# Performance work log

Hardware: AMD Instinct MI355X
Metric: run time of the kernel (lower is better)

## Reference

```python
import jax, jax.numpy as jnp
import numpy as np

H = 8          # num heads
HD = 64        # head dim
DV = 512       # values_dim
DC = 128       # coords_dim
DI = 512       # att_inner_dim
DF = 2048      # mlp inner dim


def _ln(x, g, b, eps=1e-5):
    mu = jnp.mean(x, -1, keepdims=True)
    var = jnp.mean((x - mu) ** 2, -1, keepdims=True)
    return (x - mu) * jax.lax.rsqrt(var + eps) * g + b


def _rms(x, g, eps=1e-6):
    return x * jax.lax.rsqrt(jnp.mean(x * x, -1, keepdims=True) + eps) * g


def _heads(x):  # b n (h d) -> b h n d
    b, n, _ = x.shape
    return x.reshape(b, n, H, HD).transpose(0, 2, 1, 3)


def setup_inputs() -> dict:
    key = jax.random.key(0)
    ks = iter(jax.random.split(key, 40))
    r = lambda shape, s=0.02: jax.random.normal(next(ks), shape, jnp.float32) * s
    inp = {
        'coords': jax.random.normal(next(ks), (4, 4096, DC), jnp.float32),
        'values': jax.random.normal(next(ks), (4, 4096, DV), jnp.float32),
        'Lv': jax.random.normal(next(ks), (4, 1024, DV), jnp.float32),
        'Lc': jax.random.normal(next(ks), (4, 1024, DC), jnp.float32),
        'lam': jax.random.normal(next(ks), (1,), jnp.float32),
        'lvn_g': jnp.ones((DV,)), 'lvn_b': jnp.zeros((DV,)),
        'lcn_g': jnp.ones((DC,)), 'lcn_b': jnp.zeros((DC,)),
        'ck_w': r((DC, DI)), 'ck_b': jnp.zeros((DI,)), 'ck_g': jnp.ones((DI,)),
        'cq_w': r((DC, DI)), 'cq_b': jnp.zeros((DI,)), 'cq_g': jnp.ones((DI,)),
        'vq_w': r((DV, DI)), 'vq_b': jnp.zeros((DI,)), 'vq_g': jnp.ones((DI,)),
        'vk_w': r((DV, 2 * DI)), 'vk_b': jnp.zeros((2 * DI,)),
        'op_w': r((DI, DV)), 'op_b': jnp.zeros((DV,)),
        'oln_g': jnp.ones((DV,)), 'oln_b': jnp.zeros((DV,)),
        'm1_w': r((DV, DF)), 'm1_b': jnp.zeros((DF,)),
        'm2_w': r((DF, DF)), 'm2_b': jnp.zeros((DF,)),
        'm3_w': r((DF, DV)), 'm3_b': jnp.zeros((DV,)),
    }
    return inp


def reference(coords, values, Lv, Lc, lam, lvn_g, lvn_b, lcn_g, lcn_b,
              ck_w, ck_b, ck_g, cq_w, cq_b, cq_g, vq_w, vq_b, vq_g,
              vk_w, vk_b, op_w, op_b, oln_g, oln_b,
              m1_w, m1_b, m2_w, m2_b, m3_w, m3_b):
    Lv = _ln(Lv, lvn_g, lvn_b)
    Lc = _ln(Lc, lcn_g, lcn_b)
    vk = Lv @ vk_w + vk_b                     # [b, nl, 2*DI]
    v_v, k_v = jnp.split(vk, 2, axis=-1)
    k_c = _rms(Lc @ ck_w + ck_b, ck_g)
    k_c, v_v, k_v = _heads(k_c), _heads(v_v), _heads(k_v)  # [b,h,nl,d]
    q_v = _heads(_rms(values @ vq_w + vq_b, vq_g))         # [b,h,nq,d]
    q_c = _heads(_rms(coords @ cq_w + cq_b, cq_g))
    # dual-score attention
    scores = jnp.einsum('bhnd,bhmd->bhnm', q_c, k_c) \
        + lam[0] * jnp.einsum('bhnd,bhmd->bhnm', q_v, k_v)
    scores = scores / np.float32(np.sqrt(HD))
    attn = jax.nn.softmax(scores, axis=-1)
    V_out = jnp.einsum('bhnm,bhmd->bhnd', attn, v_v)       # [b,h,nq,d]
    b, _, nq, _ = V_out.shape
    V_out = V_out.transpose(0, 2, 1, 3).reshape(b, nq, DI)
    V_out = V_out @ op_w + op_b
    # (LayerNorm, MLP) head: Linear-GELU-Linear-GELU-Linear
    h = _ln(V_out, oln_g, oln_b)
    h = jax.nn.gelu(h @ m1_w + m1_b)
    h = jax.nn.gelu(h @ m2_w + m2_b)
    return h @ m3_w + m3_b
```

## Files before the change

### kernel.cpp

```cpp
#include <hip/hip_runtime.h>
#include <cstdint>
#include <cstddef>

typedef __bf16 bf16_t;
typedef __bf16 bf16x8 __attribute__((ext_vector_type(8)));
typedef __bf16 bf16x4 __attribute__((ext_vector_type(4)));
typedef __bf16 bf16x2 __attribute__((ext_vector_type(2)));
typedef float  f32x4  __attribute__((ext_vector_type(4)));

typedef __attribute__((address_space(1))) void gvoid_t;
typedef __attribute__((address_space(3))) void lvoid_t;

__device__ __forceinline__ f32x4 mfma16(bf16x8 a, bf16x8 b, f32x4 c) {
  return __builtin_amdgcn_mfma_f32_16x16x32_bf16(a, b, c, 0, 0, 0);
}

__device__ __forceinline__ void async_copy16(const void* g, void* l) {
  __builtin_amdgcn_global_load_lds((gvoid_t*)g, (lvoid_t*)l, 16, 0, 0);
}

__device__ __forceinline__ float gelu_tanh(float x) {
  float u = 0.7978845608028654f * (x + 0.044715f * x * x * x);
  float e = exp2f(2.8853900817779268f * u);
  float t = 1.f - 2.f / (e + 1.f);
  return 0.5f * x * (1.f + t);
}

struct TransBatch {
  const float* src[8];
  bf16_t* dst[8];
  int K[8], N[8], bx[8], base[8];
};

__global__ void transpose_batch_kernel(TransBatch d) {
  int id = blockIdx.x;
  int mi = 0;
#pragma unroll
  for (int j = 1; j < 8; j++)
    if (id >= d.base[j]) mi = j;
  int local = id - d.base[mi];
  int bxw = d.bx[mi];
  int n0 = (local % bxw) * 32, k0 = (local / bxw) * 32;
  const float* in = d.src[mi];
  bf16_t* out = d.dst[mi];
  int K = d.K[mi], N = d.N[mi];

  __shared__ float t[32][33];
  int tx = threadIdx.x, ty = threadIdx.y;
#pragma unroll
  for (int i = 0; i < 4; i++)
    t[ty + i * 8][tx] = in[(size_t)(k0 + ty + i * 8) * N + n0 + tx];
  __syncthreads();
#pragma unroll
  for (int i = 0; i < 4; i++)
    out[(size_t)(n0 + ty + i * 8) * K + k0 + tx] = (bf16_t)t[tx][ty + i * 8];
}

__global__ void transpose_v_kernel(const bf16_t* __restrict__ vk, bf16_t* __restrict__ vt) {
  __shared__ bf16_t t[32][33];
  int b = blockIdx.z;
  int d0 = blockIdx.x * 32, m0 = blockIdx.y * 32;
  int tx = threadIdx.x, ty = threadIdx.y;
#pragma unroll
  for (int i = 0; i < 4; i++)
    t[ty + i * 8][tx] = vk[((size_t)b * 1024 + m0 + ty + i * 8) * 1024 + d0 + tx];
  __syncthreads();
#pragma unroll
  for (int i = 0; i < 4; i++)
    vt[((size_t)b * 512 + d0 + ty + i * 8) * 1024 + m0 + tx] = t[tx][ty + i * 8];
}

__global__ void cvt2_bf16_kernel(const float* __restrict__ a, bf16_t* __restrict__ oa, int n4a,
                                 const float* __restrict__ b, bf16_t* __restrict__ ob, int n4b) {
  int i = blockIdx.x * blockDim.x + threadIdx.x;
  const float* s;
  bf16_t* o;
  int j;
  if (i < n4a) { s = a; o = oa; j = i; }
  else { j = i - n4a; if (j >= n4b) return; s = b; o = ob; }
  float4 v = ((const float4*)s)[j];
  bf16x4 r = {(bf16_t)v.x, (bf16_t)v.y, (bf16_t)v.z, (bf16_t)v.w};
  ((bf16x4*)o)[j] = r;
}

template <int D, bool IS_RMS, typename TI>
__global__ __launch_bounds__(256) void rownorm_kernel(
    const TI* __restrict__ x, const float* __restrict__ g,
    const float* __restrict__ bb, bf16_t* __restrict__ out) {
  constexpr int V = D / 64;
  const int row = blockIdx.x * 4 + (threadIdx.x >> 6);
  const int lane = threadIdx.x & 63;
  const size_t base = (size_t)row * D + (size_t)lane * V;
  float v[V];
  if constexpr (sizeof(TI) == 2) {
    bf16x8 xv = *(const bf16x8*)(x + base);
#pragma unroll
    for (int j = 0; j < V; j++) v[j] = (float)xv[j];
  } else if constexpr (V == 8) {
    float4 a = ((const float4*)(x + base))[0];
    float4 b2 = ((const float4*)(x + base))[1];
    v[0] = a.x; v[1] = a.y; v[2] = a.z; v[3] = a.w;
    v[4] = b2.x; v[5] = b2.y; v[6] = b2.z; v[7] = b2.w;
  } else {
    float2 a = *(const float2*)(x + base);
    v[0] = a.x; v[1] = a.y;
  }
  float s = 0.f, s2 = 0.f;
#pragma unroll
  for (int j = 0; j < V; j++) { s += v[j]; s2 += v[j] * v[j]; }
#pragma unroll
  for (int o = 32; o > 0; o >>= 1) { s += __shfl_xor(s, o); s2 += __shfl_xor(s2, o); }
  float mu, rr;
  if constexpr (IS_RMS) {
    mu = 0.f;
    rr = rsqrtf(s2 * (1.f / D) + 1e-6f);
  } else {
    mu = s * (1.f / D);
    rr = rsqrtf(s2 * (1.f / D) - mu * mu + 1e-5f);
  }
  float o[V];
#pragma unroll
  for (int j = 0; j < V; j++) {
    float gv = g[lane * V + j];
    float bv;
    if constexpr (IS_RMS) bv = 0.f; else bv = bb[lane * V + j];
    o[j] = (v[j] - mu) * rr * gv + bv;
  }
  if constexpr (V == 8) {
    bf16x8 ov;
#pragma unroll
    for (int j = 0; j < 8; j++) ov[j] = (bf16_t)o[j];
    *(bf16x8*)(out + base) = ov;
  } else {
    bf16x2 ov;
    ov[0] = (bf16_t)o[0]; ov[1] = (bf16_t)o[1];
    *(bf16x2*)(out + base) = ov;
  }
}

template <int EPI>
__global__ __launch_bounds__(256, 2) void gemm_bt(
    const bf16_t* __restrict__ A, const bf16_t* __restrict__ Bt,
    const float* __restrict__ bias, void* __restrict__ outp,
    int M, int N, int K) {
  __shared__ __align__(16) bf16_t As[128 * 64];
  __shared__ __align__(16) bf16_t Bs[128 * 64];
  const int tid = threadIdx.x;
  const int lane = tid & 63, wv = tid >> 6;
  const int quad = lane >> 4, l16 = lane & 15;
  int nwg = gridDim.x * gridDim.y;
  int bid = blockIdx.y * gridDim.x + blockIdx.x;
  if (!(nwg & 7)) { int cpx = nwg >> 3; bid = (bid & 7) * cpx + (bid >> 3); }
  const int m_base = (bid / gridDim.x) * 128, n_base = (bid % gridDim.x) * 128;
  const int wm = wv & 1, wn = wv >> 1;
  f32x4 acc[4][4] = {};

  for (int k0 = 0; k0 < K; k0 += 64) {
#pragma unroll
    for (int c = 0; c < 4; c++) {
      int p = c * 256 + tid;
      int row = p >> 3;
      int gc = (p & 7) ^ (row & 7);
      async_copy16(&A[(size_t)(m_base + row) * K + k0 + gc * 8], &As[(size_t)p * 8]);
      async_copy16(&Bt[(size_t)(n_base + row) * K + k0 + gc * 8], &Bs[(size_t)p * 8]);
    }
    __syncthreads();
#pragma unroll
    for (int ks = 0; ks < 2; ks++) {
      bf16x8 af[4], bfr[4];
#pragma unroll
      for (int mi = 0; mi < 4; mi++) {
        int r = wm * 64 + mi * 16 + l16;
        int c = (ks * 4 + quad) ^ (r & 7);
        af[mi] = *(const bf16x8*)&As[(size_t)(r * 8 + c) * 8];
      }
#pragma unroll
      for (int ni = 0; ni < 4; ni++) {
        int r = wn * 64 + ni * 16 + l16;
        int c = (ks * 4 + quad) ^ (r & 7);
        bfr[ni] = *(const bf16x8*)&Bs[(size_t)(r * 8 + c) * 8];
      }
#pragma unroll
      for (int mi = 0; mi < 4; mi++)
#pragma unroll
        for (int ni = 0; ni < 4; ni++)
          acc[mi][ni] = mfma16(af[mi], bfr[ni], acc[mi][ni]);
    }
    __syncthreads();
  }

#pragma unroll
  for (int mi = 0; mi < 4; mi++) {
    int m = m_base + wm * 64 + mi * 16 + quad * 4;
#pragma unroll
    for (int ni = 0; ni < 4; ni++) {
      int n = n_base + wn * 64 + ni * 16 + l16;
      float bv = bias[n];
#pragma unroll
      for (int r2 = 0; r2 < 4; r2++) {
        float v = acc[mi][ni][r2] + bv;
        if (EPI == 2) v = gelu_tanh(v);
        if (EPI == 0) ((float*)outp)[(size_t)(m + r2) * N + n] = v;
        else          ((bf16_t*)outp)[(size_t)(m + r2) * N + n] = (bf16_t)v;
      }
    }
  }
}

#define SCHED_FENCE() __builtin_amdgcn_sched_barrier(0)

#define PHT(MM) \
  SCHED_FENCE(); \
  asm volatile("s_waitcnt lgkmcnt(0)" ::: "memory"); \
  SCHED_FENCE(); \
  __builtin_amdgcn_s_setprio(1); \
  MM; \
  __builtin_amdgcn_s_setprio(0); \
  SCHED_FENCE(); \
  __builtin_amdgcn_s_barrier(); \
  SCHED_FENCE();

#define PHT_VM(MM) \
  SCHED_FENCE(); \
  asm volatile("s_waitcnt lgkmcnt(0)" ::: "memory"); \
  SCHED_FENCE(); \
  __builtin_amdgcn_s_setprio(1); \
  MM; \
  __builtin_amdgcn_s_setprio(0); \
  SCHED_FENCE(); \
  asm volatile("s_waitcnt vmcnt(6)" ::: "memory"); \
  __builtin_amdgcn_s_barrier(); \
  SCHED_FENCE();

template <int EPI>
__global__ __launch_bounds__(512, 2) void gemm256(
    const bf16_t* __restrict__ A, const bf16_t* __restrict__ Bt,
    const float* __restrict__ bias, void* __restrict__ outp,
    int M, int N, int K) {
  __shared__ __align__(16) bf16_t As[2][256 * 64];
  __shared__ __align__(16) bf16_t Bs[2][256 * 64];
  const int tid = threadIdx.x;
  const int lane = tid & 63, wid = tid >> 6;
  const int quad = lane >> 4, l16 = lane & 15, l7 = l16 & 7;
  const int wm = wid >> 2, wn = wid & 3;
  int nwg = gridDim.x * gridDim.y;
  int bid = blockIdx.y * gridDim.x + blockIdx.x;
  if (!(nwg & 7)) { int cpx = nwg >> 3; bid = (bid & 7) * cpx + (bid >> 3); }
  const int m_base = (bid / gridDim.x) * 256, n_base = (bid % gridDim.x) * 256;
  const int nkt = K >> 6, nit = nkt >> 1;

  f32x4 acc[8][4] = {};

  const bf16_t* aB[2], * bB[2];
#pragma unroll
  for (int ks = 0; ks < 2; ks++) {
    aB[ks] = &As[0][0] + (wm * 128 + l16) * 64 + (((ks * 4 + quad) ^ l7)) * 8;
    bB[ks] = &Bs[0][0] + (wn * 64 + l16) * 64 + (((ks * 4 + quad) ^ l7)) * 8;
  }
  auto ldA = [&](int buf, int rg, bf16x8 (&af)[2][2]) {
#pragma unroll
    for (int mi = 0; mi < 2; mi++)
#pragma unroll
      for (int ks = 0; ks < 2; ks++)
        af[mi][ks] = *(const bf16x8*)(aB[ks] + buf * 16384 + rg * 2048 + mi * 1024);
  };
  auto ldB = [&](int buf, bf16x8 (&bfr)[4][2]) {
#pragma unroll
    for (int cf = 0; cf < 4; cf++)
#pragma unroll
      for (int ks = 0; ks < 2; ks++)
        bfr[cf][ks] = *(const bf16x8*)(bB[ks] + buf * 16384 + cf * 1024);
  };
  auto mm = [&](int rg, bf16x8 (&a)[2][2], bf16x8 (&b)[4][2]) {
#pragma unroll
    for (int ks = 0; ks < 2; ks++)
#pragma unroll
      for (int mi = 0; mi < 2; mi++)
#pragma unroll
        for (int cf = 0; cf < 4; cf++)
          acc[rg * 2 + mi][cf] = mfma16(a[mi][ks], b[cf][ks], acc[rg * 2 + mi][cf]);
  };

  const int rr = tid >> 3;
  const int cb = ((tid & 7) ^ (rr & 7)) * 16;
  const char* pa00 = (const char*)A + 2 * ((size_t)(m_base + 0 + rr) * K) + cb;
  const char* pa01 = (const char*)A + 2 * ((size_t)(m_base + 64 + rr) * K) + cb;
  const char* pa10 = (const char*)A + 2 * ((size_t)(m_base + 128 + rr) * K) + cb;
  const char* pa11 = (const char*)A + 2 * ((size_t)(m_base + 192 + rr) * K) + cb;
  const char* pb00 = (const char*)Bt + 2 * ((size_t)(n_base + 0 + rr) * K) + cb;
  const char* pb01 = (const char*)Bt + 2 * ((size_t)(n_base + 64 + rr) * K) + cb;
  const char* pb10 = (const char*)Bt + 2 * ((size_t)(n_base + 128 + rr) * K) + cb;
  const char* pb11 = (const char*)Bt + 2 * ((size_t)(n_base + 192 + rr) * K) + cb;
  bf16_t* dA0 = &As[0][0] + tid * 8;
  bf16_t* dB0 = &Bs[0][0] + tid * 8;
  auto stage = [&](const char*& p0, const char*& p1, bf16_t* d0) {
    async_copy16(p0, d0);
    async_copy16(p1, d0 + 4096);
    p0 += 128; p1 += 128;
  };

  stage(pb00, pb01, dB0);
  stage(pb10, pb11, dB0 + 8192);
  stage(pa00, pa01, dA0);
  stage(pa10, pa11, dA0 + 8192);
  stage(pb00, pb01, dB0 + 16384);
  stage(pb10, pb11, dB0 + 16384 + 8192);
  stage(pa00, pa01, dA0 + 16384);
  asm volatile("s_waitcnt vmcnt(6)" ::: "memory");
  SCHED_FENCE();
  __builtin_amdgcn_s_barrier();
  SCHED_FENCE();

  bf16x8 af[2][2], afn[2][2], bfr[4][2];
  for (int it = 0; it < nit; ++it) {
    ldB(0, bfr); ldA(0, 0, af);
    stage(pa10, pa11, dA0 + 16384 + 8192);
    PHT(mm(0, af, bfr));
    ldA(0, 1, af);
    stage(pb00, pb01, dB0);
    PHT(mm(1, af, bfr));
    ldA(0, 2, af); ldA(0, 3, afn);
    stage(pb10, pb11, dB0 + 8192);
    PHT(mm(2, af, bfr));
    stage(pa00, pa01, dA0);
    PHT_VM(mm(3, afn, bfr));
    ldB(1, bfr); ldA(1, 0, af);
    stage(pa10, pa11, dA0 + 8192);
    PHT(mm(0, af, bfr));
    ldA(1, 1, af);
    stage(pb00, pb01, dB0 + 16384);
    PHT(mm(1, af, bfr));
    ldA(1, 2, af); ldA(1, 3, afn);
    stage(pb10, pb11, dB0 + 16384 + 8192);
    PHT(mm(2, af, bfr));
    stage(pa00, pa01, dA0 + 16384);
    PHT_VM(mm(3, afn, bfr));
  }
  asm volatile("s_waitcnt vmcnt(0)" ::: "memory");

#pragma unroll
  for (int rf = 0; rf < 8; rf++) {
    int m = m_base + wm * 128 + rf * 16 + quad * 4;
#pragma unroll
    for (int cf = 0; cf < 4; cf++) {
      int n = n_base + wn * 64 + cf * 16 + l16;
      float bv = bias[n];
#pragma unroll
      for (int r2 = 0; r2 < 4; r2++) {
        float v = acc[rf][cf][r2] + bv;
        if (EPI == 2) v = gelu_tanh(v);
        if (EPI == 0) ((float*)outp)[(size_t)(m + r2) * N + n] = v;
        else          ((bf16_t*)outp)[(size_t)(m + r2) * N + n] = (bf16_t)v;
      }
    }
  }
}

template <int EPI>
__global__ __launch_bounds__(256, 2) void gemm64(
    const bf16_t* __restrict__ A, const bf16_t* __restrict__ Bt,
    const float* __restrict__ bias, void* __restrict__ outp,
    int M, int N, int K) {
  __shared__ __align__(16) bf16_t As[64 * 32];
  __shared__ __align__(16) bf16_t Bs[128 * 32];
  const int tid = threadIdx.x;
  const int lane = tid & 63, wv = tid >> 6;
  const int quad = lane >> 4, l16 = lane & 15;
  const int m_base = blockIdx.y * 64, n_base = blockIdx.x * 128;
  const int wm = wv & 1, wn = wv >> 1;
  f32x4 acc[2][4] = {};

  for (int k0 = 0; k0 < K; k0 += 32) {
    {
      int p = tid;
      int row = p >> 2;
      int kc = (p & 3) ^ ((row >> 1) & 3);
      async_copy16(&A[(size_t)(m_base + row) * K + k0 + kc * 8], &As[(size_t)p * 8]);
    }
#pragma unroll
    for (int c = 0; c < 2; c++) {
      int p = c * 256 + tid;
      int row = p >> 2;
      int kc = (p & 3) ^ ((row >> 1) & 3);
      async_copy16(&Bt[(size_t)(n_base + row) * K + k0 + kc * 8], &Bs[(size_t)p * 8]);
    }
    __syncthreads();
    bf16x8 af[2], bfr[4];
#pragma unroll
    for (int mi = 0; mi < 2; mi++) {
      int r = wm * 32 + mi * 16 + l16;
      int kc = quad ^ ((r >> 1) & 3);
      af[mi] = *(const bf16x8*)&As[(size_t)(r * 4 + kc) * 8];
    }
#pragma unroll
    for (int ni = 0; ni < 4; ni++) {
      int r = wn * 64 + ni * 16 + l16;
      int kc = quad ^ ((r >> 1) & 3);
      bfr[ni] = *(const bf16x8*)&Bs[(size_t)(r * 4 + kc) * 8];
    }
#pragma unroll
    for (int mi = 0; mi < 2; mi++)
#pragma unroll
      for (int ni = 0; ni < 4; ni++)
        acc[mi][ni] = mfma16(af[mi], bfr[ni], acc[mi][ni]);
    __syncthreads();
  }

#pragma unroll
  for (int mi = 0; mi < 2; mi++) {
    int m = m_base + wm * 32 + mi * 16 + quad * 4;
#pragma unroll
    for (int ni = 0; ni < 4; ni++) {
      int n = n_base + wn * 64 + ni * 16 + l16;
      float bv = bias[n];
#pragma unroll
      for (int r2 = 0; r2 < 4; r2++) {
        float v = acc[mi][ni][r2] + bv;
        if (EPI == 2) v = gelu_tanh(v);
        if (EPI == 0) ((float*)outp)[(size_t)(m + r2) * N + n] = v;
        else          ((bf16_t*)outp)[(size_t)(m + r2) * N + n] = (bf16_t)v;
      }
    }
  }
}

__global__ __launch_bounds__(256, 2) void attn_kernel(
    const bf16_t* __restrict__ qc, const bf16_t* __restrict__ qv,
    const bf16_t* __restrict__ kcb, const bf16_t* __restrict__ vkb,
    const bf16_t* __restrict__ vt, const float* __restrict__ lamp,
    bf16_t* __restrict__ vout) {
  const int b = blockIdx.z, h = blockIdx.y;
  const int tid = threadIdx.x;
  const int lane = tid & 63, wv = tid >> 6;
  const int quad = lane >> 4, l16 = lane & 15;
  const int qrow0 = blockIdx.x * 128 + wv * 32;
  const float SCL = 0.125f * 1.4426950408889634f;
  const float C1 = SCL, C2 = lamp[0] * SCL;

  __shared__ __align__(16) bf16_t kcS[64 * 64];
  __shared__ __align__(16) bf16_t kvS[64 * 64];
  __shared__ __align__(16) bf16_t vtS[64 * 64];
  __shared__ __align__(16) bf16_t sP[4][32 * 64];
  bf16_t* sPw = sP[wv];

  bf16x8 qcf[2][2], qvf[2][2];
#pragma unroll
  for (int mt = 0; mt < 2; mt++)
#pragma unroll
    for (int ks = 0; ks < 2; ks++) {
      size_t o = ((size_t)b * 4096 + qrow0 + mt * 16 + l16) * 512 + h * 64 + ks * 32 + quad * 8;
      qcf[mt][ks] = *(const bf16x8*)&qc[o];
      qvf[mt][ks] = *(const bf16x8*)&qv[o];
    }

  f32x4 O[2][4] = {};
  float ls[2][4] = {};

  for (int kb = 0; kb < 16; kb++) {
#pragma unroll
    for (int i = 0; i < 2; i++) {
      int p = i * 256 + tid;
      int row = p >> 3;
      int gc = (p & 7) ^ (row & 7);
      async_copy16(&kcb[((size_t)b * 1024 + kb * 64 + row) * 512 + h * 64 + gc * 8],
                   &kcS[(size_t)p * 8]);
      async_copy16(&vkb[((size_t)b * 1024 + kb * 64 + row) * 1024 + 512 + h * 64 + gc * 8],
                   &kvS[(size_t)p * 8]);
      async_copy16(&vt[((size_t)((b * 8 + h) * 64) + row) * 1024 + kb * 64 + gc * 8],
                   &vtS[(size_t)p * 8]);
    }
    __syncthreads();

#pragma unroll
    for (int nt = 0; nt < 4; nt++) {
      int krow = nt * 16 + l16;
      int kb8 = krow & 7;
      bf16x8 kc0 = *(const bf16x8*)&kcS[(size_t)(krow * 8 + (quad ^ kb8)) * 8];
      bf16x8 kc1 = *(const bf16x8*)&kcS[(size_t)(krow * 8 + ((4 + quad) ^ kb8)) * 8];
      bf16x8 kv0 = *(const bf16x8*)&kvS[(size_t)(krow * 8 + (quad ^ kb8)) * 8];
      bf16x8 kv1 = *(const bf16x8*)&kvS[(size_t)(krow * 8 + ((4 + quad) ^ kb8)) * 8];
#pragma unroll
      for (int mt = 0; mt < 2; mt++) {
        f32x4 sc = {};
        sc = mfma16(qcf[mt][0], kc0, sc);
        sc = mfma16(qcf[mt][1], kc1, sc);
        f32x4 sv = {};
        sv = mfma16(qvf[mt][0], kv0, sv);
        sv = mfma16(qvf[mt][1], kv1, sv);
#pragma unroll
        for (int r = 0; r < 4; r++) {
          float p = exp2f(sc[r] * C1 + sv[r] * C2);
          ls[mt][r] += p;
          int prow = mt * 16 + quad * 4 + r;
          int col = nt * 16 + l16;
          sPw[prow * 64 + (((col >> 3) ^ (prow & 7)) * 8) + (col & 7)] = (bf16_t)p;
        }
      }
    }
    asm volatile("s_waitcnt lgkmcnt(0)" ::: "memory");

#pragma unroll
    for (int ks2 = 0; ks2 < 2; ks2++) {
      bf16x8 pa[2];
#pragma unroll
      for (int mt = 0; mt < 2; mt++) {
        int prow = mt * 16 + l16;
        pa[mt] = *(const bf16x8*)&sPw[(size_t)(prow * 8 + ((ks2 * 4 + quad) ^ (prow & 7))) * 8];
      }
#pragma unroll
      for (int ntd = 0; ntd < 4; ntd++) {
        int drow = ntd * 16 + l16;
        bf16x8 vb = *(const bf16x8*)&vtS[(size_t)(drow * 8 + ((ks2 * 4 + quad) ^ (drow & 7))) * 8];
        O[0][ntd] = mfma16(pa[0], vb, O[0][ntd]);
        O[1][ntd] = mfma16(pa[1], vb, O[1][ntd]);
      }
    }
    __syncthreads();
  }

#pragma unroll
  for (int mt = 0; mt < 2; mt++) {
    float inv[4];
#pragma unroll
    for (int r = 0; r < 4; r++) {
      float v = ls[mt][r];
      v += __shfl_xor(v, 1);
      v += __shfl_xor(v, 2);
      v += __shfl_xor(v, 4);
      v += __shfl_xor(v, 8);
      inv[r] = 1.f / v;
    }
#pragma unroll
    for (int ntd = 0; ntd < 4; ntd++)
#pragma unroll
      for (int r = 0; r < 4; r++) {
        size_t o = ((size_t)b * 4096 + qrow0 + mt * 16 + quad * 4 + r) * 512 + h * 64 + ntd * 16 + l16;
        vout[o] = (bf16_t)(O[mt][ntd][r] * inv[r]);
      }
  }
}

extern "C" void kernel_launch(void* const* d_in, const int* in_sizes, int n_in,
                              void* d_out, int out_size, void* d_ws, size_t ws_size,
                              hipStream_t stream) {
  (void)in_sizes; (void)n_in; (void)out_size; (void)ws_size;
  const float* coords = (const float*)d_in[0];
  const float* values = (const float*)d_in[1];
  const float* Lv     = (const float*)d_in[2];
  const float* Lc     = (const float*)d_in[3];
  const float* lam    = (const float*)d_in[4];
  const float* lvn_g  = (const float*)d_in[5];
  const float* lvn_b  = (const float*)d_in[6];
  const float* lcn_g  = (const float*)d_in[7];
  const float* lcn_b  = (const float*)d_in[8];
  const float* ck_w = (const float*)d_in[9];  const float* ck_b = (const float*)d_in[10]; const float* ck_g = (const float*)d_in[11];
  const float* cq_w = (const float*)d_in[12]; const float* cq_b = (const float*)d_in[13]; const float* cq_g = (const float*)d_in[14];
  const float* vq_w = (const float*)d_in[15]; const float* vq_b = (const float*)d_in[16]; const float* vq_g = (const float*)d_in[17];
  const float* vk_w = (const float*)d_in[18]; const float* vk_b = (const float*)d_in[19];
  const float* op_w = (const float*)d_in[20]; const float* op_b = (const float*)d_in[21];
  const float* oln_g = (const float*)d_in[22]; const float* oln_b = (const float*)d_in[23];
  const float* m1_w = (const float*)d_in[24]; const float* m1_b = (const float*)d_in[25];
  const float* m2_w = (const float*)d_in[26]; const float* m2_b = (const float*)d_in[27];
  const float* m3_w = (const float*)d_in[28]; const float* m3_b = (const float*)d_in[29];

  char* ws = (char*)d_ws;
  size_t off = 0;
  auto alloc = [&](size_t bytes) { void* p = ws + off; off += (bytes + 255) & ~(size_t)255; return p; };

  bf16_t* wt_m1 = (bf16_t*)alloc((size_t)512 * 2048 * 2);
  bf16_t* wt_m2 = (bf16_t*)alloc((size_t)2048 * 2048 * 2);
  bf16_t* wt_m3 = (bf16_t*)alloc((size_t)2048 * 512 * 2);
  bf16_t* scr0  = (bf16_t*)alloc((size_t)16384 * 512 * 4);
  bf16_t* qv_bf = (bf16_t*)alloc((size_t)16384 * 512 * 2);
  bf16_t* qc_bf = (bf16_t*)alloc((size_t)16384 * 512 * 2);
  bf16_t* voutb = (bf16_t*)alloc((size_t)16384 * 512 * 2);
  bf16_t* h0    = (bf16_t*)alloc((size_t)16384 * 512 * 2);
  bf16_t* h1    = (bf16_t*)alloc((size_t)16384 * 2048 * 2);
  bf16_t* h2    = (bf16_t*)alloc((size_t)16384 * 2048 * 2);

  size_t ov = (size_t)((char*)h1 - ws);
  auto oalloc = [&](size_t bytes) { void* p = ws + ov; ov += (bytes + 255) & ~(size_t)255; return p; };
  bf16_t* wt_vk = (bf16_t*)oalloc((size_t)1024 * 512 * 2);
  bf16_t* wt_ck = (bf16_t*)oalloc((size_t)512 * 128 * 2);
  bf16_t* wt_cq = (bf16_t*)oalloc((size_t)512 * 128 * 2);
  bf16_t* wt_vq = (bf16_t*)oalloc((size_t)512 * 512 * 2);
  bf16_t* wt_op = (bf16_t*)oalloc((size_t)512 * 512 * 2);
  bf16_t* lv_ln = (bf16_t*)oalloc((size_t)4096 * 512 * 2);
  bf16_t* lc_ln = (bf16_t*)oalloc((size_t)4096 * 128 * 2);
  bf16_t* vkob  = (bf16_t*)oalloc((size_t)4096 * 1024 * 2);
  bf16_t* kc_b  = (bf16_t*)oalloc((size_t)4096 * 512 * 2);
  bf16_t* kc_bf = (bf16_t*)oalloc((size_t)4096 * 512 * 2);
  bf16_t* val_bf= (bf16_t*)oalloc((size_t)16384 * 512 * 2);
  bf16_t* crd_bf= (bf16_t*)oalloc((size_t)16384 * 128 * 2);
  bf16_t* vt    = (bf16_t*)oalloc((size_t)4 * 512 * 1024 * 2);

  TransBatch tb8;
  const float* srcs[8] = {vk_w, ck_w, cq_w, vq_w, op_w, m1_w, m2_w, m3_w};
  bf16_t* dsts[8] = {wt_vk, wt_ck, wt_cq, wt_vq, wt_op, wt_m1, wt_m2, wt_m3};
  int Ks[8] = {512, 128, 128, 512, 512, 512, 2048, 2048};
  int Ns[8] = {1024, 512, 512, 512, 512, 2048, 2048, 512};
  int cum = 0;
  for (int i = 0; i < 8; i++) {
    tb8.src[i] = srcs[i]; tb8.dst[i] = dsts[i];
    tb8.K[i] = Ks[i]; tb8.N[i] = Ns[i];
    tb8.bx[i] = Ns[i] / 32;
    tb8.base[i] = cum;
    cum += (Ns[i] / 32) * (Ks[i] / 32);
  }
  transpose_batch_kernel<<<cum, dim3(32, 8), 0, stream>>>(tb8);

  cvt2_bf16_kernel<<<(16384 * 512 / 4 + 16384 * 128 / 4 + 255) / 256, 256, 0, stream>>>(
      values, val_bf, 16384 * 512 / 4, coords, crd_bf, 16384 * 128 / 4);

  rownorm_kernel<512, false, float><<<1024, 256, 0, stream>>>(Lv, lvn_g, lvn_b, lv_ln);
  rownorm_kernel<128, false, float><<<1024, 256, 0, stream>>>(Lc, lcn_g, lcn_b, lc_ln);

  gemm_bt<1><<<dim3(8, 32), 256, 0, stream>>>(lv_ln, wt_vk, vk_b, vkob, 4096, 1024, 512);
  gemm64<1><<<dim3(4, 64), 256, 0, stream>>>(lc_ln, wt_ck, ck_b, kc_b, 4096, 512, 128);
  rownorm_kernel<512, true, bf16_t><<<1024, 256, 0, stream>>>(kc_b, ck_g, nullptr, kc_bf);

  gemm_bt<1><<<dim3(4, 128), 256, 0, stream>>>(val_bf, wt_vq, vq_b, scr0, 16384, 512, 512);
  rownorm_kernel<512, true, bf16_t><<<4096, 256, 0, stream>>>(scr0, vq_g, nullptr, qv_bf);
  gemm64<1><<<dim3(4, 256), 256, 0, stream>>>(crd_bf, wt_cq, cq_b, scr0, 16384, 512, 128);
  rownorm_kernel<512, true, bf16_t><<<4096, 256, 0, stream>>>(scr0, cq_g, nullptr, qc_bf);

  transpose_v_kernel<<<dim3(16, 32, 4), dim3(32, 8), 0, stream>>>(vkob, vt);

  attn_kernel<<<dim3(32, 8, 4), 256, 0, stream>>>(qc_bf, qv_bf, kc_bf, vkob, vt, lam, voutb);

  gemm_bt<1><<<dim3(4, 128), 256, 0, stream>>>(voutb, wt_op, op_b, scr0, 16384, 512, 512);
  rownorm_kernel<512, false, bf16_t><<<4096, 256, 0, stream>>>(scr0, oln_g, oln_b, h0);

  gemm_bt<2><<<dim3(16, 128), 256, 0, stream>>>(h0, wt_m1, m1_b, h1, 16384, 2048, 512);
  gemm256<2><<<dim3(8, 64), 512, 0, stream>>>(h1, wt_m2, m2_b, h2, 16384, 2048, 2048);
  gemm_bt<0><<<dim3(4, 128), 256, 0, stream>>>(h2, wt_m3, m3_b, (float*)d_out, 16384, 512, 2048);
}
```

Before: 646.6 us.

## Software-pipeline LDS fragment loads in gemm256 and use it for MLP first layer

Restructures the gemm256 main loop so each phase's LDS fragment reads for the next MFMA sub-step are issued before the current MFMA block, with the lgkmcnt wait moved after the compute. Double-buffered A/B register fragments replace the single set, and the vmcnt waits are adjusted accordingly. This lets LDS latency overlap the MFMA work instead of stalling at each phase start. The m1 GEMM (K=512) is also switched from gemm_bt to the 256x256 gemm256 kernel. Costs are higher register pressure and a short K loop for m1 that may not amortize the prologue.

```diff
diff --git a/kernel.cpp b/kernel.cpp
--- a/kernel.cpp
+++ b/kernel.cpp
@@ -207,30 +207,7 @@
   }
 }
 
-#define SCHED_FENCE() __builtin_amdgcn_sched_barrier(0)
-
-#define PHT(MM) \
-  SCHED_FENCE(); \
-  asm volatile("s_waitcnt lgkmcnt(0)" ::: "memory"); \
-  SCHED_FENCE(); \
-  __builtin_amdgcn_s_setprio(1); \
-  MM; \
-  __builtin_amdgcn_s_setprio(0); \
-  SCHED_FENCE(); \
-  __builtin_amdgcn_s_barrier(); \
-  SCHED_FENCE();
-
-#define PHT_VM(MM) \
-  SCHED_FENCE(); \
-  asm volatile("s_waitcnt lgkmcnt(0)" ::: "memory"); \
-  SCHED_FENCE(); \
-  __builtin_amdgcn_s_setprio(1); \
-  MM; \
-  __builtin_amdgcn_s_setprio(0); \
-  SCHED_FENCE(); \
-  asm volatile("s_waitcnt vmcnt(6)" ::: "memory"); \
-  __builtin_amdgcn_s_barrier(); \
-  SCHED_FENCE();
+#define SF __builtin_amdgcn_sched_barrier(0)
 
 template <int EPI>
 __global__ __launch_bounds__(512, 2) void gemm256(
@@ -247,11 +224,11 @@
   int bid = blockIdx.y * gridDim.x + blockIdx.x;
   if (!(nwg & 7)) { int cpx = nwg >> 3; bid = (bid & 7) * cpx + (bid >> 3); }
   const int m_base = (bid / gridDim.x) * 256, n_base = (bid % gridDim.x) * 256;
-  const int nkt = K >> 6, nit = nkt >> 1;
+  const int nit = K >> 7;
 
   f32x4 acc[8][4] = {};
 
-  const bf16_t* aB[2], * bB[2];
+  const bf16_t* aB[2]; const bf16_t* bB[2];
 #pragma unroll
   for (int ks = 0; ks < 2; ks++) {
     aB[ks] = &As[0][0] + (wm * 128 + l16) * 64 + (((ks * 4 + quad) ^ l7)) * 8;
@@ -307,34 +284,52 @@
   stage(pb10, pb11, dB0 + 16384 + 8192);
   stage(pa00, pa01, dA0 + 16384);
   asm volatile("s_waitcnt vmcnt(6)" ::: "memory");
-  SCHED_FENCE();
-  __builtin_amdgcn_s_barrier();
-  SCHED_FENCE();
-
-  bf16x8 af[2][2], afn[2][2], bfr[4][2];
+  SF; __builtin_amdgcn_s_barrier(); SF;
+
+  bf16x8 af0[2][2], af1[2][2], bf0[4][2], bf1[4][2];
+  ldB(0, bf0); ldA(0, 0, af0);
+
   for (int it = 0; it < nit; ++it) {
-    ldB(0, bfr); ldA(0, 0, af);
+    ldA(0, 1, af1);
     stage(pa10, pa11, dA0 + 16384 + 8192);
-    PHT(mm(0, af, bfr));
-    ldA(0, 1, af);
+    __builtin_amdgcn_s_setprio(1); mm(0, af0, bf0); __builtin_amdgcn_s_setprio(0);
+    SF; asm volatile("s_waitcnt lgkmcnt(0)" ::: "memory");
+    __builtin_amdgcn_s_barrier(); SF;
+    ldA(0, 2, af0);
     stage(pb00, pb01, dB0);
-    PHT(mm(1, af, bfr));
-    ldA(0, 2, af); ldA(0, 3, afn);
+    __builtin_amdgcn_s_setprio(1); mm(1, af1, bf0); __builtin_amdgcn_s_setprio(0);
+    SF; asm volatile("s_waitcnt lgkmcnt(0)" ::: "memory");
+    __builtin_amdgcn_s_barrier(); SF;
+    ldA(0, 3, af1);
     stage(pb10, pb11, dB0 + 8192);
-    PHT(mm(2, af, bfr));
+    __builtin_amdgcn_s_setprio(1); mm(2, af0, bf0); __builtin_amdgcn_s_setprio(0);
+    SF; asm volatile("s_waitcnt vmcnt(4) lgkmcnt(0)" ::: "memory");
+    __builtin_amdgcn_s_barrier(); SF;
+    ldB(1, bf1); ldA(1, 0, af0);
     stage(pa00, pa01, dA0);
-    PHT_VM(mm(3, afn, bfr));
-    ldB(1, bfr); ldA(1, 0, af);
+    __builtin_amdgcn_s_setprio(1); mm(3, af1, bf0); __builtin_amdgcn_s_setprio(0);
+    SF; asm volatile("s_waitcnt lgkmcnt(0)" ::: "memory");
+    __builtin_amdgcn_s_barrier(); SF;
+    ldA(1, 1, af1);
     stage(pa10, pa11, dA0 + 8192);
-    PHT(mm(0, af, bfr));
-    ldA(1, 1, af);
+    __builtin_amdgcn_s_setprio(1); mm(0, af0, bf1); __builtin_amdgcn_s_setprio(0);
+    SF; asm volatile("s_waitcnt lgkmcnt(0)" ::: "memory");
+    __builtin_amdgcn_s_barrier(); SF;
+    ldA(1, 2, af0);
     stage(pb00, pb01, dB0 + 16384);
-    PHT(mm(1, af, bfr));
-    ldA(1, 2, af); ldA(1, 3, afn);
+    __builtin_amdgcn_s_setprio(1); mm(1, af1, bf1); __builtin_amdgcn_s_setprio(0);
+    SF; asm volatile("s_waitcnt lgkmcnt(0)" ::: "memory");
+    __builtin_amdgcn_s_barrier(); SF;
+    ldA(1, 3, af1);
     stage(pb10, pb11, dB0 + 16384 + 8192);
-    PHT(mm(2, af, bfr));
+    __builtin_amdgcn_s_setprio(1); mm(2, af0, bf1); __builtin_amdgcn_s_setprio(0);
+    SF; asm volatile("s_waitcnt vmcnt(4) lgkmcnt(0)" ::: "memory");
+    __builtin_amdgcn_s_barrier(); SF;
+    ldB(0, bf0); ldA(0, 0, af0);
     stage(pa00, pa01, dA0 + 16384);
-    PHT_VM(mm(3, afn, bfr));
+    __builtin_amdgcn_s_setprio(1); mm(3, af1, bf1); __builtin_amdgcn_s_setprio(0);
+    SF; asm volatile("s_waitcnt lgkmcnt(0)" ::: "memory");
+    __builtin_amdgcn_s_barrier(); SF;
   }
   asm volatile("s_waitcnt vmcnt(0)" ::: "memory");
 
@@ -631,7 +626,7 @@
   gemm_bt<1><<<dim3(4, 128), 256, 0, stream>>>(voutb, wt_op, op_b, scr0, 16384, 512, 512);
   rownorm_kernel<512, false, bf16_t><<<4096, 256, 0, stream>>>(scr0, oln_g, oln_b, h0);
 
-  gemm_bt<2><<<dim3(16, 128), 256, 0, stream>>>(h0, wt_m1, m1_b, h1, 16384, 2048, 512);
+  gemm256<2><<<dim3(8, 64), 512, 0, stream>>>(h0, wt_m1, m1_b, h1, 16384, 2048, 512);
   gemm256<2><<<dim3(8, 64), 512, 0, stream>>>(h1, wt_m2, m2_b, h2, 16384, 2048, 2048);
   gemm_bt<0><<<dim3(4, 128), 256, 0, stream>>>(h2, wt_m3, m3_b, (float*)d_out, 16384, 512, 2048);
 }
```

New measurement: 675.0 us. 4.4% more time.
